# Kernel tuning notes

Hardware: AMD Instinct MI355X
Metric: run time of the kernel (lower is better)

The kernel has to match this reference:

```python
import jax, jax.numpy as jnp
import numpy as np

EPS = 1e-12  # torch F.normalize eps


def _l2_normalize_dim1(v):
    # torch normalize(dim=1): normalize over the POINT/EDGE axis (quirk kept faithfully)
    n = jnp.sqrt(jnp.sum(v * v, axis=1, keepdims=True))
    return v / jnp.maximum(n, EPS)


def setup_inputs() -> dict:
    key = jax.random.key(0)
    k1, k2, k3, k4 = jax.random.split(key, 4)
    B, N, E = 4, 8192, 24576
    preds = jax.random.normal(k1, (B, N, 3), dtype=jnp.float32)
    gts = jax.random.normal(k2, (B, N, 3), dtype=jnp.float32)
    normals = jax.random.normal(k3, (B, N, 3), dtype=jnp.float32)
    edges = jax.random.randint(k4, (E, 2), 0, N, dtype=jnp.int32)
    return {"preds": preds, "gts": gts, "normals": normals, "edges": edges}


def reference(preds, gts, normals, edges):
    x, y = gts, preds  # P = batch_pairwise_dist(true, pred) -> [B, Nt, Np]
    xsq = jnp.sum(x * x, axis=-1)  # [B, Nt]
    ysq = jnp.sum(y * y, axis=-1)  # [B, Np]
    zz = jnp.einsum('bnd,bmd->bnm', x, y)  # [B, Nt, Np]
    P = xsq[:, :, None] + ysq[None if False else slice(None), None, :] - 2.0 * zz
    P = xsq[:, :, None] + ysq[:, None, :] - 2.0 * zz

    mins1 = jnp.min(P, axis=1)              # [B, Np] nearest true for each pred
    loss_1 = jnp.mean(mins1)
    mins2 = jnp.min(P, axis=2)              # [B, Nt] nearest pred for each true
    nearest_idx = jnp.argmin(P, axis=2)     # [B, Nt] indices into pred points
    loss_2 = jnp.mean(mins2)
    chamfer = loss_1 + loss_2

    e0 = edges[:, 0]
    e1 = edges[:, 1]
    edge_vectors = preds[:, e0, :] - preds[:, e1, :]           # [B, E, 3]
    edge_loss = jnp.mean(jnp.sum(edge_vectors * edge_vectors, axis=2))

    # gather normals at nearest-pred index per true point, then per edge start
    normals_nearest = jnp.take_along_axis(normals, nearest_idx[:, :, None], axis=1)  # [B, Nt, 3]
    normals_edge = normals_nearest[:, e0, :]                   # [B, E, 3]

    nn = _l2_normalize_dim1(normals_edge)
    nv = _l2_normalize_dim1(edge_vectors)
    cosines = jnp.abs(jnp.sum(nn * nv, axis=2))                # [B, E]
    normal_cosine_loss = jnp.mean(cosines)

    return 30000.0 * chamfer + 240.0 * edge_loss + 200000.0 * normal_cosine_loss
```

## Files before the change

### kernel.cpp

```cpp
#include <hip/hip_runtime.h>

namespace {

constexpr int B = 4;
constexpr int N = 8192;
constexpr int E = 24576;
constexpr int BN = B * N;
constexpr int BE = B * E;
constexpr int CHUNK = 256;
constexpr int RT = 4;

typedef float f32x2 __attribute__((ext_vector_type(2)));

__device__ __forceinline__ unsigned fkey(float f) {
  unsigned b = __float_as_uint(f);
  return b ^ ((b & 0x80000000u) ? 0xFFFFFFFFu : 0x80000000u);
}
__device__ __forceinline__ float funkey(unsigned k) {
  unsigned b = k ^ ((k & 0x80000000u) ? 0x80000000u : 0xFFFFFFFFu);
  return __uint_as_float(b);
}
__device__ __forceinline__ float min3f(float a, float b, float c) {
  float d;
  asm("v_min3_f32 %0, %1, %2, %3" : "=v"(d) : "v"(a), "v"(b), "v"(c));
  return d;
}
__device__ __forceinline__ f32x2 pk_fma_vsv(f32x2 a, f32x2 bs, f32x2 c) {
  f32x2 d;
  asm("v_pk_fma_f32 %0, %1, %2, %3" : "=v"(d) : "v"(a), "s"(bs), "v"(c));
  return d;
}
__device__ __forceinline__ f32x2 pk_fma_vvv(f32x2 a, f32x2 b, f32x2 c) {
  f32x2 d;
  asm("v_pk_fma_f32 %0, %1, %2, %3" : "=v"(d) : "v"(a), "v"(b), "v"(c));
  return d;
}


__global__ __launch_bounds__(256) void prep_kernel(const float* __restrict__ preds,
                                                   const float* __restrict__ gts,
                                                   float4* __restrict__ A,
                                                   float4* __restrict__ G,
                                                   float* __restrict__ A2f,
                                                   float* __restrict__ G2f,
                                                   unsigned long long* __restrict__ m2,
                                                   unsigned* __restrict__ m1,
                                                   float* __restrict__ sums) {
  int i = blockIdx.x * 256 + threadIdx.x;
  float px = preds[3*i], py = preds[3*i+1], pz = preds[3*i+2];
  float gx = gts[3*i],   gy = gts[3*i+1],  gz = gts[3*i+2];
  float ax = -2.f*px, ay = -2.f*py, az = -2.f*pz, aw = px*px + py*py + pz*pz;
  float bx = -2.f*gx, by = -2.f*gy, bz = -2.f*gz, bw = gx*gx + gy*gy + gz*gz;
  A[i] = make_float4(ax, ay, az, aw);
  G[i] = make_float4(bx, by, bz, bw);
  int p8 = (i >> 1) * 8, l = i & 1;
  A2f[p8 + 0 + l] = ax; A2f[p8 + 2 + l] = ay; A2f[p8 + 4 + l] = az; A2f[p8 + 6 + l] = aw;
  G2f[p8 + 0 + l] = bx; G2f[p8 + 2 + l] = by; G2f[p8 + 4 + l] = bz; G2f[p8 + 6 + l] = bw;
  m2[i] = ~0ULL;
  m1[i] = 0xFFFFFFFFu;
  if (i < 32) sums[i] = 0.f;
}

__global__ __launch_bounds__(256) void pass_wave(const float4* __restrict__ A,
                                                 const float4* __restrict__ G,
                                                 const float4* __restrict__ A2,
                                                 const float4* __restrict__ G2,
                                                 unsigned long long* __restrict__ m2,
                                                 unsigned* __restrict__ m1) {
  const int wid  = __builtin_amdgcn_readfirstlane((int)(threadIdx.x >> 6));
  const int lane = threadIdx.x & 63;
  const int u    = blockIdx.x * 4 + wid;
  const int ck = u & 31, rg = (u >> 5) & 31, b = (u >> 10) & 3, which = u >> 12;
  const float4* __restrict__ R  = which ? A  : G;
  const float4* __restrict__ S2 = which ? G2 : A2;
  const float4* __restrict__ Sg = S2 + b * N + ck * CHUNK;
  const int base = ck * CHUNK;
  f32x2 x2[RT], y2[RT], z2[RT];
  float w[RT], best[RT];
#pragma unroll
  for (int i = 0; i < RT; ++i) {
    float4 r = R[b * N + rg * (64 * RT) + i * 64 + lane];
    float xx = -0.5f * r.x, yy = -0.5f * r.y, zz = -0.5f * r.z;
    x2[i] = f32x2{xx, xx}; y2[i] = f32x2{yy, yy}; z2[i] = f32x2{zz, zz};
    w[i] = r.w; best[i] = 3.4e38f;
  }
  if (which == 0) {
    int wjj[RT];
#pragma unroll
    for (int i = 0; i < RT; ++i) wjj[i] = 0;
#pragma unroll 8
    for (int jr = 0; jr < CHUNK / 2; ++jr) {
      float4 qa = Sg[2*jr], qb = Sg[2*jr + 1];
      f32x2 qx = f32x2{qa.x, qa.y}, qy = f32x2{qa.z, qa.w};
      f32x2 qz = f32x2{qb.x, qb.y}, qw = f32x2{qb.z, qb.w};
#pragma unroll
      for (int i = 0; i < RT; ++i) {
        f32x2 t = pk_fma_vsv(z2[i], qz, qw);
        t = pk_fma_vsv(y2[i], qy, t);
        t = pk_fma_vsv(x2[i], qx, t);
        float m = min3f(best[i], t.x, t.y);
        wjj[i] = (m < best[i]) ? 2*jr : wjj[i];
        best[i] = m;
      }
    }
#pragma unroll
    for (int i = 0; i < RT; ++i) {
      float4 qa = Sg[wjj[i]], qb = Sg[wjj[i] + 1];
      f32x2 t = pk_fma_vvv(z2[i], f32x2{qb.x, qb.y}, f32x2{qb.z, qb.w});
      t = pk_fma_vvv(y2[i], f32x2{qa.z, qa.w}, t);
      t = pk_fma_vvv(x2[i], f32x2{qa.x, qa.y}, t);
      const int idx = base + wjj[i] + ((t.x <= t.y) ? 0 : 1);
      const int gi = b * N + rg * (64 * RT) + i * 64 + lane;
      float d = w[i] + best[i];
      atomicMin(&m2[gi], ((unsigned long long)fkey(d) << 32) | (unsigned)idx);
    }
  } else {
#pragma unroll 8
    for (int jr = 0; jr < CHUNK / 2; ++jr) {
      float4 qa = Sg[2*jr], qb = Sg[2*jr + 1];
      f32x2 qx = f32x2{qa.x, qa.y}, qy = f32x2{qa.z, qa.w};
      f32x2 qz = f32x2{qb.x, qb.y}, qw = f32x2{qb.z, qb.w};
#pragma unroll
      for (int i = 0; i < RT; ++i) {
        f32x2 t = pk_fma_vsv(z2[i], qz, qw);
        t = pk_fma_vsv(y2[i], qy, t);
        t = pk_fma_vsv(x2[i], qx, t);
        best[i] = min3f(best[i], t.x, t.y);
      }
    }
#pragma unroll
    for (int i = 0; i < RT; ++i) {
      const int gi = b * N + rg * (64 * RT) + i * 64 + lane;
      atomicMin(&m1[gi], fkey(w[i] + best[i]));
    }
  }
}

__device__ __forceinline__ float block_sum(float v, float* ws) {
#pragma unroll
  for (int o = 32; o; o >>= 1) v += __shfl_down(v, o, 64);
  __syncthreads();
  if ((threadIdx.x & 63) == 0) ws[threadIdx.x >> 6] = v;
  __syncthreads();
  return ws[0] + ws[1] + ws[2] + ws[3];
}

__global__ __launch_bounds__(256) void post_kernel(const unsigned long long* __restrict__ m2,
                                                   const unsigned* __restrict__ m1,
                                                   unsigned* __restrict__ nidx,
                                                   float* __restrict__ sums) {
  __shared__ float ws[4];
  int i = blockIdx.x * 256 + threadIdx.x;
  unsigned long long p = m2[i];
  nidx[i] = (unsigned)p;
  float d2 = funkey((unsigned)(p >> 32));
  float d1 = funkey(m1[i]);
  float s2 = block_sum(d2, ws);
  float s1 = block_sum(d1, ws);
  if (threadIdx.x == 0) { atomicAdd(&sums[1], s2); atomicAdd(&sums[0], s1); }
}

__global__ __launch_bounds__(256) void edge1_kernel(const float* __restrict__ preds,
                                                    const float* __restrict__ normals,
                                                    const int* __restrict__ edges,
                                                    const unsigned* __restrict__ nidx,
                                                    float* __restrict__ ev,
                                                    float* __restrict__ sums) {
  __shared__ float ws[4][6];
  const int b = blockIdx.y;
  const int e = blockIdx.x * 256 + threadIdx.x;
  const int wid = threadIdx.x >> 6, lane = threadIdx.x & 63;
  int e0 = edges[2*e], e1 = edges[2*e+1];
  const float* pb = preds   + 3*(size_t)b*N;
  const float* nb = normals + 3*(size_t)b*N;
  float vx = pb[3*e0]   - pb[3*e1];
  float vy = pb[3*e0+1] - pb[3*e1+1];
  float vz = pb[3*e0+2] - pb[3*e1+2];
  unsigned ni = nidx[b*N + e0];
  float nx = nb[3*ni], ny = nb[3*ni+1], nz = nb[3*ni+2];
  const int be = b * E + e;
  ev[0*BE + be] = vx; ev[1*BE + be] = vy; ev[2*BE + be] = vz;
  ev[3*BE + be] = nx; ev[4*BE + be] = ny; ev[5*BE + be] = nz;
  float v[6] = {nx*nx, ny*ny, nz*nz, vx*vx, vy*vy, vz*vz};
#pragma unroll
  for (int k = 0; k < 6; ++k)
#pragma unroll
    for (int o = 32; o; o >>= 1) v[k] += __shfl_down(v[k], o, 64);
  if (lane == 0) {
#pragma unroll
    for (int k = 0; k < 6; ++k) ws[wid][k] = v[k];
  }
  __syncthreads();
  if (threadIdx.x < 6) {
    const int k = threadIdx.x;
    float t = ws[0][k] + ws[1][k] + ws[2][k] + ws[3][k];
    atomicAdd(&sums[(k < 3 ? 3 + k : 12 + k) + b*3], t);
  }
}

__global__ __launch_bounds__(256) void edge2_kernel(const float* __restrict__ ev,
                                                    float* __restrict__ sums) {
  __shared__ float ws[4];
  const int b = blockIdx.y;
  const int e = blockIdx.x * 256 + threadIdx.x;
  const int be = b * E + e;
  float vx = ev[0*BE + be], vy = ev[1*BE + be], vz = ev[2*BE + be];
  float nx = ev[3*BE + be], ny = ev[4*BE + be], nz = ev[5*BE + be];
  float inn0 = 1.f / fmaxf(sqrtf(sums[3  + b*3 + 0]), 1e-12f);
  float inn1 = 1.f / fmaxf(sqrtf(sums[3  + b*3 + 1]), 1e-12f);
  float inn2 = 1.f / fmaxf(sqrtf(sums[3  + b*3 + 2]), 1e-12f);
  float inv0 = 1.f / fmaxf(sqrtf(sums[15 + b*3 + 0]), 1e-12f);
  float inv1 = 1.f / fmaxf(sqrtf(sums[15 + b*3 + 1]), 1e-12f);
  float inv2 = 1.f / fmaxf(sqrtf(sums[15 + b*3 + 2]), 1e-12f);
  float c = fabsf(nx*inn0*vx*inv0 + ny*inn1*vy*inv1 + nz*inn2*vz*inv2);
#pragma unroll
  for (int o = 32; o; o >>= 1) c += __shfl_down(c, o, 64);
  if ((threadIdx.x & 63) == 0) ws[threadIdx.x >> 6] = c;
  __syncthreads();
  if (threadIdx.x == 0) atomicAdd(&sums[2], ws[0] + ws[1] + ws[2] + ws[3]);
}

__global__ void final_kernel(const float* __restrict__ sums, float* __restrict__ out) {
  if (threadIdx.x == 0 && blockIdx.x == 0) {
    float esum = 0.f;
#pragma unroll
    for (int i = 0; i < 12; ++i) esum += sums[15 + i];
    float chamfer   = (sums[0] + sums[1]) * (1.f / (float)BN);
    float edge_loss = esum * (1.f / (float)(B * E));
    float ncl       = sums[2] * (1.f / (float)(B * E));
    out[0] = 30000.f * chamfer + 240.f * edge_loss + 200000.f * ncl;
  }
}

}

extern "C" void kernel_launch(void* const* d_in, const int* in_sizes, int n_in,
                              void* d_out, int out_size, void* d_ws, size_t ws_size,
                              hipStream_t stream) {
  (void)in_sizes; (void)n_in; (void)out_size; (void)ws_size;
  const float* preds   = (const float*)d_in[0];
  const float* gts     = (const float*)d_in[1];
  const float* normals = (const float*)d_in[2];
  const int*   edges   = (const int*)d_in[3];
  char* ws = (char*)d_ws;
  float4*             A    = (float4*)(ws);
  float4*             G    = (float4*)(ws + 0x080000);
  float4*             A2   = (float4*)(ws + 0x100000);
  float4*             G2   = (float4*)(ws + 0x180000);
  unsigned long long* m2   = (unsigned long long*)(ws + 0x200000);
  unsigned*           m1   = (unsigned*)(ws + 0x240000);
  unsigned*           nidx = (unsigned*)(ws + 0x260000);
  float*              sums = (float*)(ws + 0x280000);
  float*              ev   = (float*)(ws + 0x281000);
  float* out = (float*)d_out;

  prep_kernel<<<dim3(BN/256), 256, 0, stream>>>(preds, gts, A, G, (float*)A2, (float*)G2,
                                                m2, m1, sums);
  pass_wave<<<dim3(2048), 256, 0, stream>>>(A, G, A2, G2, m2, m1);
  post_kernel<<<dim3(BN/256), 256, 0, stream>>>(m2, m1, nidx, sums);
  edge1_kernel<<<dim3(E/256, B), 256, 0, stream>>>(preds, normals, edges, nidx, ev, sums);
  edge2_kernel<<<dim3(E/256, B), 256, 0, stream>>>(ev, sums);
  final_kernel<<<1, 64, 0, stream>>>(sums, out);
}
```

Baseline: 74.15 us.

## Fuse post, edge and final kernels into one grid-barrier tail kernel

Replaces the four tail kernels (post, edge1, edge2, final) with one 512-block kernel. Edge blocks and chamfer-reduction blocks run side by side, then software grid barriers on atomic counters separate the normalization and final phases. This removes the launch gaps and the intermediate ev and nidx buffers, because edge values stay in registers across the barrier. It also reorders the pass_wave work index so both directions are interleaved in neighbouring waves. The barrier assumes all 512 blocks are resident at the same time, and spinning on the counters adds some cost.

Result: slower. 274.3 us (+270.0%).

```diff
diff --git a/kernel.cpp b/kernel.cpp
--- a/kernel.cpp
+++ b/kernel.cpp
@@ -6,7 +6,6 @@
 constexpr int N = 8192;
 constexpr int E = 24576;
 constexpr int BN = B * N;
-constexpr int BE = B * E;
 constexpr int CHUNK = 256;
 constexpr int RT = 4;
 
@@ -70,7 +69,7 @@
   const int wid  = __builtin_amdgcn_readfirstlane((int)(threadIdx.x >> 6));
   const int lane = threadIdx.x & 63;
   const int u    = blockIdx.x * 4 + wid;
-  const int ck = u & 31, rg = (u >> 5) & 31, b = (u >> 10) & 3, which = u >> 12;
+  const int which = u & 1, ck = (u >> 1) & 31, rg = (u >> 6) & 31, b = (u >> 11) & 3;
   const float4* __restrict__ R  = which ? A  : G;
   const float4* __restrict__ S2 = which ? G2 : A2;
   const float4* __restrict__ Sg = S2 + b * N + ck * CHUNK;
@@ -136,98 +135,107 @@
   }
 }
 
-__device__ __forceinline__ float block_sum(float v, float* ws) {
-#pragma unroll
-  for (int o = 32; o; o >>= 1) v += __shfl_down(v, o, 64);
+__device__ __forceinline__ void gbar(unsigned* c, unsigned n) {
+  __threadfence();
   __syncthreads();
-  if ((threadIdx.x & 63) == 0) ws[threadIdx.x >> 6] = v;
+  if (threadIdx.x == 0) {
+    atomicAdd(c, 1u);
+    while (atomicAdd(c, 0u) < n) __builtin_amdgcn_s_sleep(2);
+  }
   __syncthreads();
-  return ws[0] + ws[1] + ws[2] + ws[3];
-}
-
-__global__ __launch_bounds__(256) void post_kernel(const unsigned long long* __restrict__ m2,
+  __threadfence();
+}
+
+__global__ __launch_bounds__(256) void tail_kernel(const float* __restrict__ preds,
+                                                   const float* __restrict__ normals,
+                                                   const int* __restrict__ edges,
+                                                   const unsigned long long* __restrict__ m2,
                                                    const unsigned* __restrict__ m1,
-                                                   unsigned* __restrict__ nidx,
-                                                   float* __restrict__ sums) {
-  __shared__ float ws[4];
-  int i = blockIdx.x * 256 + threadIdx.x;
-  unsigned long long p = m2[i];
-  nidx[i] = (unsigned)p;
-  float d2 = funkey((unsigned)(p >> 32));
-  float d1 = funkey(m1[i]);
-  float s2 = block_sum(d2, ws);
-  float s1 = block_sum(d1, ws);
-  if (threadIdx.x == 0) { atomicAdd(&sums[1], s2); atomicAdd(&sums[0], s1); }
-}
-
-__global__ __launch_bounds__(256) void edge1_kernel(const float* __restrict__ preds,
-                                                    const float* __restrict__ normals,
-                                                    const int* __restrict__ edges,
-                                                    const unsigned* __restrict__ nidx,
-                                                    float* __restrict__ ev,
-                                                    float* __restrict__ sums) {
+                                                   float* __restrict__ sums,
+                                                   float* __restrict__ out) {
   __shared__ float ws[4][6];
-  const int b = blockIdx.y;
-  const int e = blockIdx.x * 256 + threadIdx.x;
-  const int wid = threadIdx.x >> 6, lane = threadIdx.x & 63;
-  int e0 = edges[2*e], e1 = edges[2*e+1];
-  const float* pb = preds   + 3*(size_t)b*N;
-  const float* nb = normals + 3*(size_t)b*N;
-  float vx = pb[3*e0]   - pb[3*e1];
-  float vy = pb[3*e0+1] - pb[3*e1+1];
-  float vz = pb[3*e0+2] - pb[3*e1+2];
-  unsigned ni = nidx[b*N + e0];
-  float nx = nb[3*ni], ny = nb[3*ni+1], nz = nb[3*ni+2];
-  const int be = b * E + e;
-  ev[0*BE + be] = vx; ev[1*BE + be] = vy; ev[2*BE + be] = vz;
-  ev[3*BE + be] = nx; ev[4*BE + be] = ny; ev[5*BE + be] = nz;
-  float v[6] = {nx*nx, ny*ny, nz*nz, vx*vx, vy*vy, vz*vz};
-#pragma unroll
-  for (int k = 0; k < 6; ++k)
-#pragma unroll
-    for (int o = 32; o; o >>= 1) v[k] += __shfl_down(v[k], o, 64);
-  if (lane == 0) {
-#pragma unroll
-    for (int k = 0; k < 6; ++k) ws[wid][k] = v[k];
-  }
-  __syncthreads();
-  if (threadIdx.x < 6) {
-    const int k = threadIdx.x;
-    float t = ws[0][k] + ws[1][k] + ws[2][k] + ws[3][k];
-    atomicAdd(&sums[(k < 3 ? 3 + k : 12 + k) + b*3], t);
-  }
-}
-
-__global__ __launch_bounds__(256) void edge2_kernel(const float* __restrict__ ev,
-                                                    float* __restrict__ sums) {
-  __shared__ float ws[4];
-  const int b = blockIdx.y;
-  const int e = blockIdx.x * 256 + threadIdx.x;
-  const int be = b * E + e;
-  float vx = ev[0*BE + be], vy = ev[1*BE + be], vz = ev[2*BE + be];
-  float nx = ev[3*BE + be], ny = ev[4*BE + be], nz = ev[5*BE + be];
-  float inn0 = 1.f / fmaxf(sqrtf(sums[3  + b*3 + 0]), 1e-12f);
-  float inn1 = 1.f / fmaxf(sqrtf(sums[3  + b*3 + 1]), 1e-12f);
-  float inn2 = 1.f / fmaxf(sqrtf(sums[3  + b*3 + 2]), 1e-12f);
-  float inv0 = 1.f / fmaxf(sqrtf(sums[15 + b*3 + 0]), 1e-12f);
-  float inv1 = 1.f / fmaxf(sqrtf(sums[15 + b*3 + 1]), 1e-12f);
-  float inv2 = 1.f / fmaxf(sqrtf(sums[15 + b*3 + 2]), 1e-12f);
-  float c = fabsf(nx*inn0*vx*inv0 + ny*inn1*vy*inv1 + nz*inn2*vz*inv2);
-#pragma unroll
-  for (int o = 32; o; o >>= 1) c += __shfl_down(c, o, 64);
-  if ((threadIdx.x & 63) == 0) ws[threadIdx.x >> 6] = c;
-  __syncthreads();
-  if (threadIdx.x == 0) atomicAdd(&sums[2], ws[0] + ws[1] + ws[2] + ws[3]);
-}
-
-__global__ void final_kernel(const float* __restrict__ sums, float* __restrict__ out) {
-  if (threadIdx.x == 0 && blockIdx.x == 0) {
+  __shared__ float nrm[12];
+  const int tid = threadIdx.x;
+  const int wid = tid >> 6, lane = tid & 63;
+  unsigned* cnt = (unsigned*)(sums + 28);
+  int b = 0;
+  float vx = 0.f, vy = 0.f, vz = 0.f, nx = 0.f, ny = 0.f, nz = 0.f;
+  if (blockIdx.x < 384) {
+    b = blockIdx.x / 96;
+    const int e = (blockIdx.x % 96) * 256 + tid;
+    int e0 = edges[2*e], e1 = edges[2*e+1];
+    const float* pb = preds   + 3*(size_t)b*N;
+    const float* nb = normals + 3*(size_t)b*N;
+    vx = pb[3*e0]   - pb[3*e1];
+    vy = pb[3*e0+1] - pb[3*e1+1];
+    vz = pb[3*e0+2] - pb[3*e1+2];
+    unsigned ni = (unsigned)m2[b*N + e0];
+    nx = nb[3*ni]; ny = nb[3*ni+1]; nz = nb[3*ni+2];
+    float v[6] = {nx*nx, ny*ny, nz*nz, vx*vx, vy*vy, vz*vz};
+#pragma unroll
+    for (int k = 0; k < 6; ++k)
+#pragma unroll
+      for (int o = 32; o; o >>= 1) v[k] += __shfl_down(v[k], o, 64);
+    if (lane == 0) {
+#pragma unroll
+      for (int k = 0; k < 6; ++k) ws[wid][k] = v[k];
+    }
+    __syncthreads();
+    if (tid < 6) {
+      const int k = tid;
+      float t = ws[0][k] + ws[1][k] + ws[2][k] + ws[3][k];
+      atomicAdd(&sums[(k < 3 ? 3 + k : 12 + k) + b*3], t);
+    }
+  } else {
+    int i = (blockIdx.x - 384) * 256 + tid;
+    float d2 = funkey((unsigned)(m2[i] >> 32));
+    float d1 = funkey(m1[i]);
+#pragma unroll
+    for (int o = 32; o; o >>= 1) { d2 += __shfl_down(d2, o, 64); d1 += __shfl_down(d1, o, 64); }
+    if (lane == 0) { ws[wid][0] = d2; ws[wid][1] = d1; }
+    __syncthreads();
+    if (tid == 0) {
+      atomicAdd(&sums[1], ws[0][0] + ws[1][0] + ws[2][0] + ws[3][0]);
+      atomicAdd(&sums[0], ws[0][1] + ws[1][1] + ws[2][1] + ws[3][1]);
+    }
+  }
+  gbar(&cnt[0], 512);
+  if (blockIdx.x < 384) {
+    if (tid < 12) {
+      int k = tid;
+      nrm[k] = atomicAdd(&sums[(k < 6 ? 3 + (k % 3) : 12 + (k % 3)) + (k < 6 ? 0 : 0) +
+                               ((k % 6) < 3 ? 0 : 9) + b*3 + 0], 0.f);
+    }
+    __syncthreads();
+    if (tid < 6) {
+      int k = tid;
+      nrm[k] = atomicAdd(&sums[(k < 3 ? 3 + k : 12 + k) + b*3], 0.f);
+    }
+    __syncthreads();
+    float inn0 = 1.f / fmaxf(sqrtf(nrm[0]), 1e-12f);
+    float inn1 = 1.f / fmaxf(sqrtf(nrm[1]), 1e-12f);
+    float inn2 = 1.f / fmaxf(sqrtf(nrm[2]), 1e-12f);
+    float inv0 = 1.f / fmaxf(sqrtf(nrm[3]), 1e-12f);
+    float inv1 = 1.f / fmaxf(sqrtf(nrm[4]), 1e-12f);
+    float inv2 = 1.f / fmaxf(sqrtf(nrm[5]), 1e-12f);
+    float c = fabsf(nx*inn0*vx*inv0 + ny*inn1*vy*inv1 + nz*inn2*vz*inv2);
+#pragma unroll
+    for (int o = 32; o; o >>= 1) c += __shfl_down(c, o, 64);
+    __syncthreads();
+    if (lane == 0) ws[wid][0] = c;
+    __syncthreads();
+    if (tid == 0) atomicAdd(&sums[2], ws[0][0] + ws[1][0] + ws[2][0] + ws[3][0]);
+  }
+  gbar(&cnt[1], 512);
+  if (blockIdx.x == 0 && tid == 0) {
     float esum = 0.f;
 #pragma unroll
-    for (int i = 0; i < 12; ++i) esum += sums[15 + i];
-    float chamfer   = (sums[0] + sums[1]) * (1.f / (float)BN);
+    for (int i = 0; i < 12; ++i) esum += atomicAdd(&sums[15 + i], 0.f);
+    float s0 = atomicAdd(&sums[0], 0.f), s1 = atomicAdd(&sums[1], 0.f);
+    float s2 = atomicAdd(&sums[2], 0.f);
+    float chamfer   = (s0 + s1) * (1.f / (float)BN);
     float edge_loss = esum * (1.f / (float)(B * E));
-    float ncl       = sums[2] * (1.f / (float)(B * E));
+    float ncl       = s2 * (1.f / (float)(B * E));
     out[0] = 30000.f * chamfer + 240.f * edge_loss + 200000.f * ncl;
   }
 }
@@ -249,16 +257,11 @@
   float4*             G2   = (float4*)(ws + 0x180000);
   unsigned long long* m2   = (unsigned long long*)(ws + 0x200000);
   unsigned*           m1   = (unsigned*)(ws + 0x240000);
-  unsigned*           nidx = (unsigned*)(ws + 0x260000);
-  float*              sums = (float*)(ws + 0x280000);
-  float*              ev   = (float*)(ws + 0x281000);
+  float*              sums = (float*)(ws + 0x260000);
   float* out = (float*)d_out;
 
   prep_kernel<<<dim3(BN/256), 256, 0, stream>>>(preds, gts, A, G, (float*)A2, (float*)G2,
                                                 m2, m1, sums);
   pass_wave<<<dim3(2048), 256, 0, stream>>>(A, G, A2, G2, m2, m1);
-  post_kernel<<<dim3(BN/256), 256, 0, stream>>>(m2, m1, nidx, sums);
-  edge1_kernel<<<dim3(E/256, B), 256, 0, stream>>>(preds, normals, edges, nidx, ev, sums);
-  edge2_kernel<<<dim3(E/256, B), 256, 0, stream>>>(ev, sums);
-  final_kernel<<<1, 64, 0, stream>>>(sums, out);
-}
+  tail_kernel<<<dim3(512), 256, 0, stream>>>(preds, normals, edges, m2, m1, sums, out);
+}
```
